# Kernel optimization log

Measured on AMD Instinct MI355X. Metric: run time of the kernel, lower is better.

The kernel has to match this reference:

```python
import jax, jax.numpy as jnp
import numpy as np

B = 131072
N_NUM = 48
N_CAT = 16
N_CLASSES = 32
NUM_IDX = np.arange(0, 48)
CAT_IDX = np.arange(48, 64)


def setup_inputs() -> dict:
    key = jax.random.key(0)
    ks = jax.random.split(key, 9)
    num_x = jax.random.normal(ks[0], (B, N_NUM), dtype=jnp.float32)
    cat_x = jax.random.randint(ks[1], (B, N_CAT), 0, N_CLASSES).astype(jnp.float32)
    inputs = jnp.concatenate([num_x, cat_x], axis=1)  # [B, 64]
    s = 0.5
    W0 = jax.random.normal(ks[2], (N_NUM, 1, 40), dtype=jnp.float32) * s
    b0 = jax.random.normal(ks[3], (N_NUM, 40), dtype=jnp.float32) * 0.1
    W1 = jax.random.normal(ks[4], (N_NUM, 40, 20), dtype=jnp.float32) * s
    b1 = jax.random.normal(ks[5], (N_NUM, 20), dtype=jnp.float32) * 0.1
    W2 = jax.random.normal(ks[6], (N_NUM, 20, 1), dtype=jnp.float32) * s
    b2 = jax.random.normal(ks[7], (N_NUM, 1), dtype=jnp.float32) * 0.1
    class_bias = jax.random.normal(ks[8], (N_CAT, N_CLASSES), dtype=jnp.float32) * 0.1
    return {"inputs": inputs, "W0": W0, "b0": b0, "W1": W1, "b1": b1,
            "W2": W2, "b2": b2, "class_bias": class_bias}


def reference(inputs, W0, b0, W1, b1, W2, b2, class_bias):
    # --- numerical branch: n_subnets independent tiny MLPs (TensorLayer) ---
    # xs: [n_subnets, B, 1]
    xs = jnp.transpose(inputs[:, NUM_IDX])[:, :, None]
    xs = jax.nn.relu(jnp.einsum('nbi,nio->nbo', xs, W0) + b0[:, None, :])
    xs = jax.nn.relu(jnp.einsum('nbi,nio->nbo', xs, W1) + b1[:, None, :])
    num_out = jnp.einsum('nbi,nio->nbo', xs, W2) + b2[:, None, :]  # [n, B, 1]
    num_out = jnp.transpose(num_out[:, :, 0])  # [B, n_subnets]
    # --- categorical branch: one_hot @ class_bias == gather (global_bias=0) ---
    idx = inputs[:, CAT_IDX].astype(jnp.int32)  # [B, n_cat]
    cat_out = class_bias[jnp.arange(N_CAT)[None, :], idx]  # [B, n_cat]
    out = jnp.zeros((inputs.shape[0], inputs.shape[1]), dtype=jnp.float32)
    out = out.at[:, NUM_IDX].set(num_out)
    out = out.at[:, CAT_IDX].set(cat_out)
    return out
```

## Files before the change

kernel.cpp:

```cpp
#include <hip/hip_runtime.h>


constexpr int NCOLS = 64;
constexpr int NNUM  = 48;
constexpr int NCAT  = 16;
constexpr int NCLS  = 32;
constexpr int H0N   = 40;
constexpr int H1N   = 20;

#define BLOCK 256
#define RG    64
#define TPAD  20

__global__ __launch_bounds__(BLOCK, 6)
void gam_kernel(const float* __restrict__ inp,
                const float* __restrict__ W0, const float* __restrict__ b0,
                const float* __restrict__ W1, const float* __restrict__ b1,
                const float* __restrict__ W2, const float* __restrict__ b2,
                const float* __restrict__ cbias,
                float* __restrict__ out)
{
    __shared__ float tile[RG * TPAD];
    __shared__ float cb[NCAT * NCLS];

    const int lane = threadIdx.x & 63;
    const int wv   = __builtin_amdgcn_readfirstlane(threadIdx.x >> 6);
    const int fg   = blockIdx.y;
    const long long row = (long long)blockIdx.x * RG + lane;
    const float* __restrict__ rowp = inp + row * NCOLS;

    if (fg == 3) {
        for (int i = threadIdx.x; i < NCAT * NCLS; i += BLOCK) cb[i] = cbias[i];
    }
    __syncthreads();

    if (fg < 3) {
        const int fbase = fg * 16 + wv * 4;
        #pragma unroll 1
        for (int ff = 0; ff < 4; ++ff) {
            const int f = fbase + ff;
            const float x = rowp[f];
            const float* __restrict__ w0  = W0 + f * H0N;
            const float* __restrict__ bb0 = b0 + f * H0N;
            const float* __restrict__ w1  = W1 + f * H0N * H1N;
            const float* __restrict__ bb1 = b1 + f * H1N;
            const float* __restrict__ w2  = W2 + f * H1N;

            float h1[H1N];
            #pragma unroll
            for (int o = 0; o < H1N; ++o) h1[o] = bb1[o];

            #pragma unroll
            for (int k = 0; k < H0N; ++k) {
                const float h0k = fmaxf(fmaf(x, w0[k], bb0[k]), 0.0f);
                #pragma unroll
                for (int o = 0; o < H1N; ++o)
                    h1[o] = fmaf(h0k, w1[k * H1N + o], h1[o]);
            }

            float acc = b2[f];
            #pragma unroll
            for (int o = 0; o < H1N; ++o)
                acc = fmaf(fmaxf(h1[o], 0.0f), w2[o], acc);

            tile[lane * TPAD + wv * 4 + ff] = acc;
        }
    } else {
        const int jbase = wv * 4;
        #pragma unroll 1
        for (int ff = 0; ff < 4; ++ff) {
            const int j = jbase + ff;
            const float x = rowp[NNUM + j];
            const int idx = (int)x;
            tile[lane * TPAD + j] = cb[j * NCLS + idx];
        }
    }

    __syncthreads();

    const int r  = threadIdx.x >> 2;
    const int c4 = threadIdx.x & 3;
    const float* src = &tile[r * TPAD + c4 * 4];
    float4 v = make_float4(src[0], src[1], src[2], src[3]);
    float* gout = out + ((long long)blockIdx.x * RG + r) * NCOLS + fg * 16 + c4 * 4;
    *reinterpret_cast<float4*>(gout) = v;
}

extern "C" void kernel_launch(void* const* d_in, const int* in_sizes, int n_in,
                              void* d_out, int out_size, void* d_ws, size_t ws_size,
                              hipStream_t stream) {
    const float* inp   = (const float*)d_in[0];
    const float* W0    = (const float*)d_in[1];
    const float* b0    = (const float*)d_in[2];
    const float* W1    = (const float*)d_in[3];
    const float* b1    = (const float*)d_in[4];
    const float* W2    = (const float*)d_in[5];
    const float* b2    = (const float*)d_in[6];
    const float* cbias = (const float*)d_in[7];
    float* out = (float*)d_out;

    const int nrows = 131072;
    dim3 grid(nrows / RG, 4);
    dim3 block(BLOCK);
    gam_kernel<<<grid, block, 0, stream>>>(inp, W0, b0, W1, b1, W2, b2, cbias, out);
}
```

Before: 249.5 us.

## Stage per-feature weights in LDS and split features across more blocks

The grid's y dimension grows from 4 to 13 groups, so each block handles 4 features with one feature per wavefront instead of 16 features with 4 per wave. The block first copies those features' W0/b0/W1/b1/W2/b2 into shared memory, and the MLP inner loop reads weights from LDS rather than through scalar global loads. Launch bounds rise to 8 waves per SIMD. The cost is many more blocks, each paying its own weight-staging load and barrier, narrow 4-float output stores per row, and LDS broadcast reads in place of scalar-register operands in the FMA loop.

```diff
diff --git a/kernel.cpp b/kernel.cpp
--- a/kernel.cpp
+++ b/kernel.cpp
@@ -10,9 +10,13 @@
 
 #define BLOCK 256
 #define RG    64
-#define TPAD  20
+#define FPB   4
+#define TP    5
+#define TP16  20
 
-__global__ __launch_bounds__(BLOCK, 6)
+#define SM_FLOATS 4008
+
+__global__ __launch_bounds__(BLOCK, 8)
 void gam_kernel(const float* __restrict__ inp,
                 const float* __restrict__ W0, const float* __restrict__ b0,
                 const float* __restrict__ W1, const float* __restrict__ b1,
@@ -20,70 +24,95 @@
                 const float* __restrict__ cbias,
                 float* __restrict__ out)
 {
-    __shared__ float tile[RG * TPAD];
-    __shared__ float cb[NCAT * NCLS];
+    __shared__ float smem[SM_FLOATS];
 
-    const int lane = threadIdx.x & 63;
-    const int wv   = __builtin_amdgcn_readfirstlane(threadIdx.x >> 6);
-    const int fg   = blockIdx.y;
-    const long long row = (long long)blockIdx.x * RG + lane;
-    const float* __restrict__ rowp = inp + row * NCOLS;
+    const int t    = threadIdx.x;
+    const int lane = t & 63;
+    const int wv   = __builtin_amdgcn_readfirstlane(t >> 6);
+    const int yg   = blockIdx.y;
+    const long long row0 = (long long)blockIdx.x * RG;
+    const float* __restrict__ rowp = inp + (row0 + lane) * NCOLS;
 
-    if (fg == 3) {
-        for (int i = threadIdx.x; i < NCAT * NCLS; i += BLOCK) cb[i] = cbias[i];
-    }
-    __syncthreads();
+    if (yg < 12) {
+        float* w1s  = smem;
+        float* w0s  = smem + 3200;
+        float* b0s  = smem + 3360;
+        float* b1s  = smem + 3520;
+        float* w2s  = smem + 3600;
+        float* b2s  = smem + 3680;
+        float* tile = smem + 3684;
 
-    if (fg < 3) {
-        const int fbase = fg * 16 + wv * 4;
-        #pragma unroll 1
-        for (int ff = 0; ff < 4; ++ff) {
-            const int f = fbase + ff;
-            const float x = rowp[f];
-            const float* __restrict__ w0  = W0 + f * H0N;
-            const float* __restrict__ bb0 = b0 + f * H0N;
-            const float* __restrict__ w1  = W1 + f * H0N * H1N;
-            const float* __restrict__ bb1 = b1 + f * H1N;
-            const float* __restrict__ w2  = W2 + f * H1N;
+        const int fbase = yg * FPB;
 
-            float h1[H1N];
+        {
+            const float4* s = reinterpret_cast<const float4*>(W1 + fbase * H0N * H1N);
+            float4* d = reinterpret_cast<float4*>(w1s);
             #pragma unroll
-            for (int o = 0; o < H1N; ++o) h1[o] = bb1[o];
+            for (int j = 0; j < (FPB * H0N * H1N / 4) / BLOCK + 1; ++j) {
+                int i = j * BLOCK + t;
+                if (i < FPB * H0N * H1N / 4) d[i] = s[i];
+            }
+        }
+        if (t < FPB * H0N / 4) {
+            reinterpret_cast<float4*>(w0s)[t] = reinterpret_cast<const float4*>(W0 + fbase * H0N)[t];
+            reinterpret_cast<float4*>(b0s)[t] = reinterpret_cast<const float4*>(b0 + fbase * H0N)[t];
+        }
+        if (t < FPB * H1N / 4) {
+            reinterpret_cast<float4*>(b1s)[t] = reinterpret_cast<const float4*>(b1 + fbase * H1N)[t];
+            reinterpret_cast<float4*>(w2s)[t] = reinterpret_cast<const float4*>(W2 + fbase * H1N)[t];
+        }
+        if (t < FPB) b2s[t] = b2[fbase + t];
+        __syncthreads();
 
-            #pragma unroll
-            for (int k = 0; k < H0N; ++k) {
-                const float h0k = fmaxf(fmaf(x, w0[k], bb0[k]), 0.0f);
-                #pragma unroll
-                for (int o = 0; o < H1N; ++o)
-                    h1[o] = fmaf(h0k, w1[k * H1N + o], h1[o]);
-            }
+        const int f = fbase + wv;
+        const float x = rowp[f];
+        const float* __restrict__ wf1 = w1s + wv * H0N * H1N;
+        const float* __restrict__ wf0 = w0s + wv * H0N;
+        const float* __restrict__ bf0 = b0s + wv * H0N;
 
-            float acc = b2[f];
+        float h1[H1N];
+        #pragma unroll
+        for (int o = 0; o < H1N; ++o) h1[o] = b1s[wv * H1N + o];
+
+        #pragma unroll
+        for (int k = 0; k < H0N; ++k) {
+            const float h0k = fmaxf(fmaf(x, wf0[k], bf0[k]), 0.0f);
             #pragma unroll
             for (int o = 0; o < H1N; ++o)
-                acc = fmaf(fmaxf(h1[o], 0.0f), w2[o], acc);
+                h1[o] = fmaf(h0k, wf1[k * H1N + o], h1[o]);
+        }
 
-            tile[lane * TPAD + wv * 4 + ff] = acc;
-        }
+        float acc = b2s[wv];
+        #pragma unroll
+        for (int o = 0; o < H1N; ++o)
+            acc = fmaf(fmaxf(h1[o], 0.0f), w2s[wv * H1N + o], acc);
+
+        tile[lane * TP + wv] = acc;
+        __syncthreads();
+
+        const int r = t >> 2, c = t & 3;
+        out[(row0 + r) * NCOLS + fbase + c] = tile[r * TP + c];
     } else {
+        float* cb     = smem;
+        float* tile16 = smem + 512;
+
+        for (int i = t; i < NCAT * NCLS; i += BLOCK) cb[i] = cbias[i];
+        __syncthreads();
+
         const int jbase = wv * 4;
-        #pragma unroll 1
+        #pragma unroll
         for (int ff = 0; ff < 4; ++ff) {
             const int j = jbase + ff;
-            const float x = rowp[NNUM + j];
-            const int idx = (int)x;
-            tile[lane * TPAD + j] = cb[j * NCLS + idx];
+            const int idx = (int)rowp[NNUM + j];
+            tile16[lane * TP16 + j] = cb[j * NCLS + idx];
         }
+        __syncthreads();
+
+        const int r = t >> 2, c4 = t & 3;
+        const float* src = &tile16[r * TP16 + c4 * 4];
+        float4 v = make_float4(src[0], src[1], src[2], src[3]);
+        *reinterpret_cast<float4*>(out + (row0 + r) * NCOLS + NNUM + c4 * 4) = v;
     }
-
-    __syncthreads();
-
-    const int r  = threadIdx.x >> 2;
-    const int c4 = threadIdx.x & 3;
-    const float* src = &tile[r * TPAD + c4 * 4];
-    float4 v = make_float4(src[0], src[1], src[2], src[3]);
-    float* gout = out + ((long long)blockIdx.x * RG + r) * NCOLS + fg * 16 + c4 * 4;
-    *reinterpret_cast<float4*>(gout) = v;
 }
 
 extern "C" void kernel_launch(void* const* d_in, const int* in_sizes, int n_in,
@@ -100,7 +129,7 @@
     float* out = (float*)d_out;
 
     const int nrows = 131072;
-    dim3 grid(nrows / RG, 4);
+    dim3 grid(nrows / RG, 13);
     dim3 block(BLOCK);
     gam_kernel<<<grid, block, 0, stream>>>(inp, W0, b0, W1, b1, W2, b2, cbias, out);
 }
```

New measurement: 251.4 us. No clear change (+0.7%).

## Process four rows per thread per feature group to amortize weight loads

Applied to the files above, without the earlier changes.

Restructures the kernel so each block handles 6 numeric features plus 2 categorical columns for 1024 rows, with every thread computing 4 rows at once. Each weight load is reused across 4 independent FMA chains, cutting the scalar weight-load overhead per FLOP and balancing categorical work across all blocks instead of giving it a dedicated group of blocks. The LDS transpose tile is removed and outputs are written directly with strided scalar stores. The cost is higher register pressure (occupancy hint lowered from 6 to 4), less coalesced stores and a smaller grid of 1024 blocks.

```diff
diff --git a/kernel.cpp b/kernel.cpp
--- a/kernel.cpp
+++ b/kernel.cpp
@@ -3,16 +3,16 @@
 
 constexpr int NCOLS = 64;
 constexpr int NNUM  = 48;
-constexpr int NCAT  = 16;
 constexpr int NCLS  = 32;
 constexpr int H0N   = 40;
 constexpr int H1N   = 20;
 
 #define BLOCK 256
-#define RG    64
-#define TPAD  20
+#define FPB   6
+#define NRG   128
+#define RPW   256
 
-__global__ __launch_bounds__(BLOCK, 6)
+__global__ __launch_bounds__(BLOCK, 4)
 void gam_kernel(const float* __restrict__ inp,
                 const float* __restrict__ W0, const float* __restrict__ b0,
                 const float* __restrict__ W1, const float* __restrict__ b1,
@@ -20,70 +20,102 @@
                 const float* __restrict__ cbias,
                 float* __restrict__ out)
 {
-    __shared__ float tile[RG * TPAD];
-    __shared__ float cb[NCAT * NCLS];
+    __shared__ float cb[2 * NCLS];
 
-    const int lane = threadIdx.x & 63;
-    const int wv   = __builtin_amdgcn_readfirstlane(threadIdx.x >> 6);
-    const int fg   = blockIdx.y;
-    const long long row = (long long)blockIdx.x * RG + lane;
-    const float* __restrict__ rowp = inp + row * NCOLS;
+    const int t    = threadIdx.x;
+    const int lane = t & 63;
+    const int wv   = t >> 6;
+    const int fg   = blockIdx.x >> 7;
+    const int rg   = blockIdx.x & (NRG - 1);
+    const int rowbase = rg * (4 * RPW) + wv * RPW + lane;
 
-    if (fg == 3) {
-        for (int i = threadIdx.x; i < NCAT * NCLS; i += BLOCK) cb[i] = cbias[i];
-    }
+    if (t < 2 * NCLS) cb[t] = cbias[2 * fg * NCLS + t];
     __syncthreads();
 
-    if (fg < 3) {
-        const int fbase = fg * 16 + wv * 4;
-        #pragma unroll 1
-        for (int ff = 0; ff < 4; ++ff) {
-            const int f = fbase + ff;
-            const float x = rowp[f];
-            const float* __restrict__ w0  = W0 + f * H0N;
-            const float* __restrict__ bb0 = b0 + f * H0N;
-            const float* __restrict__ w1  = W1 + f * H0N * H1N;
-            const float* __restrict__ bb1 = b1 + f * H1N;
-            const float* __restrict__ w2  = W2 + f * H1N;
+    const float* __restrict__ rp = inp + (long long)rowbase * NCOLS;
 
-            float h1[H1N];
+    int cidx0[4], cidx1[4];
+    #pragma unroll
+    for (int q = 0; q < 4; ++q) {
+        cidx0[q] = (int)rp[q * 64 * NCOLS + NNUM + 2 * fg + 0];
+        cidx1[q] = (int)rp[q * 64 * NCOLS + NNUM + 2 * fg + 1];
+    }
+
+    float xc0 = rp[0 * 64 * NCOLS + fg * FPB];
+    float xc1 = rp[1 * 64 * NCOLS + fg * FPB];
+    float xc2 = rp[2 * 64 * NCOLS + fg * FPB];
+    float xc3 = rp[3 * 64 * NCOLS + fg * FPB];
+
+    #pragma unroll 1
+    for (int j = 0; j < FPB; ++j) {
+        const int f = fg * FPB + j;
+        const float* __restrict__ w0f = W0 + f * H0N;
+        const float* __restrict__ b0f = b0 + f * H0N;
+        const float* __restrict__ w1f = W1 + f * H0N * H1N;
+        const float* __restrict__ b1f = b1 + f * H1N;
+        const float* __restrict__ w2f = W2 + f * H1N;
+
+        float xn0 = 0.f, xn1 = 0.f, xn2 = 0.f, xn3 = 0.f;
+        if (j < FPB - 1) {
+            xn0 = rp[0 * 64 * NCOLS + f + 1];
+            xn1 = rp[1 * 64 * NCOLS + f + 1];
+            xn2 = rp[2 * 64 * NCOLS + f + 1];
+            xn3 = rp[3 * 64 * NCOLS + f + 1];
+        }
+
+        float h10[H1N], h11[H1N], h12[H1N], h13[H1N];
+        #pragma unroll
+        for (int o = 0; o < H1N; ++o) {
+            const float bv = b1f[o];
+            h10[o] = bv; h11[o] = bv; h12[o] = bv; h13[o] = bv;
+        }
+
+        #pragma unroll 10
+        for (int k = 0; k < H0N; ++k) {
+            const float w0k = w0f[k], b0k = b0f[k];
+            const float a0 = fmaxf(fmaf(xc0, w0k, b0k), 0.f);
+            const float a1 = fmaxf(fmaf(xc1, w0k, b0k), 0.f);
+            const float a2 = fmaxf(fmaf(xc2, w0k, b0k), 0.f);
+            const float a3 = fmaxf(fmaf(xc3, w0k, b0k), 0.f);
+            const float* __restrict__ wk = w1f + k * H1N;
             #pragma unroll
-            for (int o = 0; o < H1N; ++o) h1[o] = bb1[o];
+            for (int o = 0; o < H1N; ++o) {
+                const float w = wk[o];
+                h10[o] = fmaf(a0, w, h10[o]);
+                h11[o] = fmaf(a1, w, h11[o]);
+                h12[o] = fmaf(a2, w, h12[o]);
+                h13[o] = fmaf(a3, w, h13[o]);
+            }
+        }
 
-            #pragma unroll
-            for (int k = 0; k < H0N; ++k) {
-                const float h0k = fmaxf(fmaf(x, w0[k], bb0[k]), 0.0f);
-                #pragma unroll
-                for (int o = 0; o < H1N; ++o)
-                    h1[o] = fmaf(h0k, w1[k * H1N + o], h1[o]);
-            }
+        const float b2v = b2[f];
+        float acc0 = b2v, acc1 = b2v, acc2 = b2v, acc3 = b2v;
+        #pragma unroll
+        for (int o = 0; o < H1N; ++o) {
+            const float w = w2f[o];
+            acc0 = fmaf(fmaxf(h10[o], 0.f), w, acc0);
+            acc1 = fmaf(fmaxf(h11[o], 0.f), w, acc1);
+            acc2 = fmaf(fmaxf(h12[o], 0.f), w, acc2);
+            acc3 = fmaf(fmaxf(h13[o], 0.f), w, acc3);
+        }
 
-            float acc = b2[f];
-            #pragma unroll
-            for (int o = 0; o < H1N; ++o)
-                acc = fmaf(fmaxf(h1[o], 0.0f), w2[o], acc);
+        float* op = out + (long long)rowbase * NCOLS + f;
+        op[0 * 64 * NCOLS] = acc0;
+        op[1 * 64 * NCOLS] = acc1;
+        op[2 * 64 * NCOLS] = acc2;
+        op[3 * 64 * NCOLS] = acc3;
 
-            tile[lane * TPAD + wv * 4 + ff] = acc;
-        }
-    } else {
-        const int jbase = wv * 4;
-        #pragma unroll 1
-        for (int ff = 0; ff < 4; ++ff) {
-            const int j = jbase + ff;
-            const float x = rowp[NNUM + j];
-            const int idx = (int)x;
-            tile[lane * TPAD + j] = cb[j * NCLS + idx];
+        xc0 = xn0; xc1 = xn1; xc2 = xn2; xc3 = xn3;
+    }
+
+    {
+        float* op = out + (long long)rowbase * NCOLS + NNUM + 2 * fg;
+        #pragma unroll
+        for (int q = 0; q < 4; ++q) {
+            op[q * 64 * NCOLS + 0] = cb[cidx0[q]];
+            op[q * 64 * NCOLS + 1] = cb[NCLS + cidx1[q]];
         }
     }
-
-    __syncthreads();
-
-    const int r  = threadIdx.x >> 2;
-    const int c4 = threadIdx.x & 3;
-    const float* src = &tile[r * TPAD + c4 * 4];
-    float4 v = make_float4(src[0], src[1], src[2], src[3]);
-    float* gout = out + ((long long)blockIdx.x * RG + r) * NCOLS + fg * 16 + c4 * 4;
-    *reinterpret_cast<float4*>(gout) = v;
 }
 
 extern "C" void kernel_launch(void* const* d_in, const int* in_sizes, int n_in,
@@ -99,8 +131,7 @@
     const float* cbias = (const float*)d_in[7];
     float* out = (float*)d_out;
 
-    const int nrows = 131072;
-    dim3 grid(nrows / RG, 4);
+    dim3 grid(8 * NRG);
     dim3 block(BLOCK);
     gam_kernel<<<grid, block, 0, stream>>>(inp, W0, b0, W1, b1, W2, b2, cbias, out);
 }
```

After: 374.0 us. +49.9%, slower.
